# Kernel optimization log

Hardware: AMD Instinct MI355X
Metric: run time of the kernel (lower is better)

## Reference

```python
import jax, jax.numpy as jnp
import numpy as np

B, N, T, D, H, NE = 8, 128, 49, 4, 256, 2  # batch, nodes, timesteps, dims, hidden, edge types


def _mlp(x, w1, b1, w2, b2):
    # NRI-style 2-layer MLP with ELU activations (dropout=0, batch_norm off)
    h = jax.nn.elu(x @ w1 + b1)
    return jax.nn.elu(h @ w2 + b2)


def setup_inputs() -> dict:
    key = jax.random.key(0)
    ks = jax.random.split(key, 11)
    # fully-connected graph without self loops -> E = N*(N-1)
    off = ~np.eye(N, dtype=bool)
    recv_idx, send_idx = np.nonzero(off)
    eye = np.eye(N, dtype=np.float32)
    rec_rel = jnp.asarray(eye[recv_idx])   # [E, N] one-hot receivers
    send_rel = jnp.asarray(eye[send_idx])  # [E, N] one-hot senders
    x = jax.random.normal(ks[0], (B, N, T, D), jnp.float32)

    def lin(k, fi, fo):
        kw, kb = jax.random.split(k)
        return (0.02 * jax.random.normal(kw, (fi, fo), jnp.float32),
                0.02 * jax.random.normal(kb, (fo,), jnp.float32))

    F = T * D
    n1w1, n1b1 = lin(ks[1], F, H)
    n1w2, n1b2 = lin(ks[2], H, H)
    e1w1, e1b1 = lin(ks[3], 2 * H, H)
    e1w2, e1b2 = lin(ks[4], H, H)
    n2w1, n2b1 = lin(ks[5], H, H)
    n2w2, n2b2 = lin(ks[6], H, H)
    e2w1, e2b1 = lin(ks[7], 3 * H, H)
    e2w2, e2b2 = lin(ks[8], H, H)
    ow, ob = lin(ks[9], H, NE)
    return dict(x=x, rec_rel=rec_rel, send_rel=send_rel,
                n1w1=n1w1, n1b1=n1b1, n1w2=n1w2, n1b2=n1b2,
                e1w1=e1w1, e1b1=e1b1, e1w2=e1w2, e1b2=e1b2,
                n2w1=n2w1, n2b1=n2b1, n2w2=n2w2, n2b2=n2b2,
                e2w1=e2w1, e2b1=e2b1, e2w2=e2w2, e2b2=e2b2,
                ow=ow, ob=ob)


def reference(x, rec_rel, send_rel,
              n1w1, n1b1, n1w2, n1b2,
              e1w1, e1b1, e1w2, e1b2,
              n2w1, n2b1, n2w2, n2b2,
              e2w1, e2b1, e2w2, e2b2,
              ow, ob):
    b, n = x.shape[0], x.shape[1]
    h = x.reshape(b, n, -1)                         # [B, N, T*D]
    h = _mlp(h, n1w1, n1b1, n1w2, n1b2)             # node_emd 1 -> [B, N, H]
    r = jnp.einsum('en,bnf->bef', rec_rel, h)       # gather receivers [B, E, H]
    s = jnp.einsum('en,bnf->bef', send_rel, h)      # gather senders  [B, E, H]
    e = _mlp(jnp.concatenate([r, s], -1), e1w1, e1b1, e1w2, e1b2)  # edge_emd 1
    x_skip = e                                      # '@' skip connection
    agg = jnp.einsum('en,bef->bnf', rec_rel, e)     # aggregate sum -> [B, N, H]
    h = _mlp(agg, n2w1, n2b1, n2w2, n2b2)           # node_emd 2
    r = jnp.einsum('en,bnf->bef', rec_rel, h)
    s = jnp.einsum('en,bnf->bef', send_rel, h)
    e = jnp.concatenate([r, s, x_skip], -1)         # pairwise concat + residual cat
    e = _mlp(e, e2w1, e2b1, e2w2, e2b2)             # edge_emd 2 (final)
    return e @ ow + ob                              # [B, E, n_edge_types]
```

## Files before the change

### kernel.cpp

```cpp
#include <hip/hip_runtime.h>
#include <hip/hip_bf16.h>

typedef unsigned short ushort_t;
typedef short bf16x8 __attribute__((ext_vector_type(8)));
typedef float f32x4 __attribute__((ext_vector_type(4)));

#define B_ 8
#define N_ 128
#define E_ 16256
#define BE 130048

__device__ __forceinline__ float eluf(float x) {
    return x > 0.0f ? x : __expf(x) - 1.0f;
}
__device__ __forceinline__ ushort_t f2bf(float f) {
    union { float f; unsigned u; } v; v.f = f;
    return (ushort_t)((v.u + 0x7fffu + ((v.u >> 16) & 1u)) >> 16);
}

__device__ __forceinline__ void glds16(void* lds, const void* g) {
    __builtin_amdgcn_global_load_lds(
        (const __attribute__((address_space(1))) unsigned int*)g,
        (__attribute__((address_space(3))) unsigned int*)lds, 16, 0, 0);
}

__device__ __forceinline__ void img32_elem(const float* __restrict__ w,
                                           ushort_t* __restrict__ img, int i) {
    int c = i >> 13;  int r = i & 8191;
    int n = r >> 5;   int jq = r & 31;
    int quad = jq >> 3, j = jq & 7;
    int kc = quad ^ ((n >> 1) & 3);
    int k = c * 32 + kc * 8 + j;
    img[i] = f2bf(w[(size_t)k * 256 + n]);
}
__device__ __forceinline__ void img64_elem(const float* __restrict__ w,
                                           ushort_t* __restrict__ img, int i) {
    int c = i >> 14;  int r = i & 16383;
    int n = r >> 6;   int wdx = r & 63;
    int up = wdx >> 3, j = wdx & 7;
    int u = up ^ (n & 7);
    int k = c * 64 + u * 8 + j;
    img[i] = f2bf(w[(size_t)k * 256 + n]);
}
__device__ __forceinline__ void img128_elem(const float* __restrict__ w,
                                            ushort_t* __restrict__ img, int i) {
    int c = i >> 15;  int r = i & 32767;
    int n = r >> 7;   int wdx = r & 127;
    int up = wdx >> 3, j = wdx & 7;
    int u = up ^ (n & 15);
    int k = c * 128 + u * 8 + j;
    img[i] = f2bf(w[(size_t)k * 256 + n]);
}
__device__ __forceinline__ void img128_pad(const float* __restrict__ w,
                                           ushort_t* __restrict__ img, int i, int Kreal) {
    int c = i >> 15;  int r = i & 32767;
    int n = r >> 7;   int wdx = r & 127;
    int up = wdx >> 3, j = wdx & 7;
    int u = up ^ (n & 15);
    int k = c * 128 + u * 8 + j;
    img[i] = (k < Kreal) ? f2bf(w[(size_t)k * 256 + n]) : (ushort_t)0;
}

__global__ __launch_bounds__(256) void wprep_all(
    const float* __restrict__ n1w1, ushort_t* __restrict__ s0,
    const float* __restrict__ n1w2, ushort_t* __restrict__ s1,
    const float* __restrict__ e1w1, ushort_t* __restrict__ s2, ushort_t* __restrict__ s3,
    const float* __restrict__ n2w1, ushort_t* __restrict__ s4,
    const float* __restrict__ n2w2, ushort_t* __restrict__ s5,
    const float* __restrict__ e2w1, ushort_t* __restrict__ s6, ushort_t* __restrict__ s7,
    ushort_t* __restrict__ s8,
    const float* __restrict__ e1w2, ushort_t* __restrict__ s9,
    const float* __restrict__ e2w2, ushort_t* __restrict__ s10)
{
    int gid = blockIdx.x * 256 + threadIdx.x;
    int img = gid >> 16, r = gid & 65535;
    switch (img) {
        case 0:  img128_pad (n1w1, s0, r, 196); break;
        case 1:  img128_elem(n1w2, s1, r); break;
        case 2:  img128_elem(e1w1, s2, r); break;
        case 3:  img128_elem(e1w1 + 65536, s3, r); break;
        case 4:  img128_elem(n2w1, s4, r); break;
        case 5:  img128_elem(n2w2, s5, r); break;
        case 6:  img128_elem(e2w1, s6, r); break;
        case 7:  img128_elem(e2w1 + 65536, s7, r); break;
        case 8:  img64_elem (e2w1 + 131072, s8, r); break;
        case 9:  img32_elem (e1w2, s9, r); break;
        default: img32_elem (e2w2, s10, r); break;
    }
}

template<bool TWOIN>
__global__ __launch_bounds__(256, 1) void node_fused(
    const float* __restrict__ in0, const float* __restrict__ in1,
    const ushort_t* __restrict__ iw1, const float* __restrict__ b1,
    const ushort_t* __restrict__ iw2, const float* __restrict__ b2,
    const ushort_t* __restrict__ ipr, const ushort_t* __restrict__ ips,
    const float* __restrict__ bE,
    float* __restrict__ P)
{
    extern __shared__ char smem[];
    const int t = threadIdx.x;
    const int wid = t >> 6, lane = t & 63, lr = lane & 15, lg = lane >> 4;
    const int r0 = blockIdx.x * 32;

    float bias1[4], bias2[4], biasP[4];
    #pragma unroll
    for (int f = 0; f < 4; ++f) {
        int col = wid * 64 + f * 16 + lr;
        bias1[f] = b1[col];
        bias2[f] = b2[col];
        biasP[f] = 0.5f * bE[col];
    }

    f32x4 acc[2][4];
    #pragma unroll
    for (int m = 0; m < 2; ++m)
        #pragma unroll
        for (int f = 0; f < 4; ++f) acc[m][f] = f32x4{0.f, 0.f, 0.f, 0.f};

    auto stageW = [&](const ushort_t* img, int c, int p) {
        const char* src = (const char*)img + (size_t)c * 65536 + wid * 16384 + lane * 16;
        char* dst = smem + 16384 + p * 65536 + wid * 16384;
        #pragma unroll
        for (int it = 0; it < 16; ++it) glds16(dst + it * 1024, src + it * 1024);
    };

    int cc = 0;
    auto runGemm = [&](const ushort_t* img, const ushort_t* nimg) {
        for (int c = 0; c < 2; ++c) {
            const int p = cc & 1;
            if (c + 1 < 2)  stageW(img, 1, p ^ 1);
            else if (nimg)  stageW(nimg, 0, p ^ 1);
            const char* Wp = smem + 16384 + p * 65536;
            #pragma unroll
            for (int ks = 0; ks < 4; ++ks) {
                const int c32 = c * 4 + ks;
                bf16x8 a[2], b[4];
                const int qh = ((c32 * 4 + lg) ^ (lr & 7)) << 4;
                #pragma unroll
                for (int m = 0; m < 2; ++m)
                    a[m] = *(const bf16x8*)(smem + (m * 16 + lr) * 512 + qh);
                #pragma unroll
                for (int f = 0; f < 4; ++f)
                    b[f] = *(const bf16x8*)(Wp + (wid * 64 + f * 16 + lr) * 256 + (((ks * 4 + lg) ^ lr) << 4));
                #pragma unroll
                for (int m = 0; m < 2; ++m)
                    #pragma unroll
                    for (int f = 0; f < 4; ++f)
                        acc[m][f] = __builtin_amdgcn_mfma_f32_16x16x32_bf16(a[m], b[f], acc[m][f], 0, 0, 0);
            }
            __syncthreads();
            ++cc;
        }
    };

    auto transition = [&](const float* bv) {
        #pragma unroll
        for (int m = 0; m < 2; ++m)
            #pragma unroll
            for (int f = 0; f < 4; ++f) {
                const int col = wid * 64 + f * 16 + lr;
                const int ch = col >> 3;
                #pragma unroll
                for (int r = 0; r < 4; ++r) {
                    const int row = m * 16 + lg * 4 + r;
                    float v = eluf(acc[m][f][r] + bv[f]);
                    *(ushort_t*)(smem + row * 512 + ((ch ^ (row & 7)) << 4) + ((col & 7) << 1)) = f2bf(v);
                }
                acc[m][f] = f32x4{0.f, 0.f, 0.f, 0.f};
            }
        __syncthreads();
    };

    auto pwrite = [&](int half) {
        #pragma unroll
        for (int m = 0; m < 2; ++m)
            #pragma unroll
            for (int f = 0; f < 4; ++f) {
                const int col = wid * 64 + f * 16 + lr;
                #pragma unroll
                for (int r = 0; r < 4; ++r) {
                    const int row = m * 16 + lg * 4 + r;
                    P[(size_t)(r0 + row) * 512 + half * 256 + col] = acc[m][f][r] + biasP[f];
                }
                acc[m][f] = f32x4{0.f, 0.f, 0.f, 0.f};
            }
    };

    stageW(iw1, 0, 0);
    for (int idx = t; idx < 32 * 128; idx += 256) {
        const int row = idx >> 7;
        const int c0 = (idx & 127) * 2;
        float v0, v1;
        if (TWOIN) {
            const float* pa = in0 + (size_t)(r0 + row) * 256;
            const float* pb = in1 + (size_t)(r0 + row) * 256;
            v0 = pa[c0] + pb[c0];
            v1 = pa[c0 + 1] + pb[c0 + 1];
        } else {
            const float* pa = in0 + (size_t)(r0 + row) * 196;
            v0 = (c0 < 196) ? pa[c0] : 0.f;
            v1 = (c0 + 1 < 196) ? pa[c0 + 1] : 0.f;
        }
        unsigned u = (unsigned)f2bf(v0) | ((unsigned)f2bf(v1) << 16);
        const int ch = c0 >> 3;
        *(unsigned*)(smem + row * 512 + ((ch ^ (row & 7)) << 4) + (c0 & 7) * 2) = u;
    }
    __syncthreads();

    runGemm(iw1, iw2);
    transition(bias1);
    runGemm(iw2, ipr);
    transition(bias2);
    runGemm(ipr, ips);
    pwrite(0);
    runGemm(ips, nullptr);
    pwrite(1);
}

__global__ __launch_bounds__(512, 2) void edge1_kernel(
    const float* __restrict__ P1,
    const ushort_t* __restrict__ wimg, const float* __restrict__ bias,
    ushort_t* __restrict__ eout,
    float* __restrict__ aggp0, float* __restrict__ aggp1)
{
    extern __shared__ char smem[];
    const int t = threadIdx.x;
    const int wid = t >> 6, lane = t & 63, lr = lane & 15, lg = lane >> 4;
    const int wr = wid >> 1, wc = wid & 1;
    const int q4 = (lg ^ ((lr >> 1) & 3)) << 4;
    const int blockRow = blockIdx.x * 256;

    auto stageW = [&](int c, int p) {
        const char* src = (const char*)wimg + (size_t)c * 16384 + wid * 2048 + lane * 16;
        char* dst = smem + 131072 + p * 16384 + wid * 2048;
        glds16(dst, src);
        glds16(dst + 1024, src + 1024);
    };

    float biasA[8];
    #pragma unroll
    for (int f = 0; f < 8; ++f) biasA[f] = bias[wc * 128 + f * 16 + lr];

    f32x4 acc[4][8];
    #pragma unroll
    for (int m = 0; m < 4; ++m)
        #pragma unroll
        for (int f = 0; f < 8; ++f) acc[m][f] = f32x4{0.f, 0.f, 0.f, 0.f};

    stageW(0, 0);
    #pragma unroll 4
    for (int j = 0; j < 32; ++j) {
        const int row = wid * 32 + j;
        const int rg = blockRow + row;
        const int b = rg / E_; const int e = rg - b * E_;
        const int rcv = e / 127; const int kk = e - rcv * 127;
        const int snd = kk + (kk >= rcv ? 1 : 0);
        const float4 vr = *(const float4*)(P1 + (size_t)(b * N_ + rcv) * 512 + lane * 4);
        const float4 vs = *(const float4*)(P1 + (size_t)(b * N_ + snd) * 512 + 256 + lane * 4);
        unsigned u0 = (unsigned)f2bf(eluf(vr.x + vs.x)) | ((unsigned)f2bf(eluf(vr.y + vs.y)) << 16);
        unsigned u1 = (unsigned)f2bf(eluf(vr.z + vs.z)) | ((unsigned)f2bf(eluf(vr.w + vs.w)) << 16);
        const int byte = row * 512 + ((((lane >> 1) ^ (row & 7))) << 4) + (lane & 1) * 8;
        *(uint2*)(smem + byte) = make_uint2(u0, u1);
    }
    __syncthreads();

    for (int c = 0; c < 8; ++c) {
        const int p = c & 1;
        if (c < 7) stageW(c + 1, p ^ 1);
        const char* Wp = smem + 131072 + p * 16384;
        bf16x8 a[4], b[8];
        const int qh = ((c * 4 + lg) ^ (lr & 7)) << 4;
        #pragma unroll
        for (int m = 0; m < 4; ++m)
            a[m] = *(const bf16x8*)(smem + (wr * 64 + m * 16 + lr) * 512 + qh);
        #pragma unroll
        for (int f = 0; f < 8; ++f)
            b[f] = *(const bf16x8*)(Wp + (wc * 128 + f * 16 + lr) * 64 + q4);
        #pragma unroll
        for (int m = 0; m < 4; ++m)
            #pragma unroll
            for (int f = 0; f < 8; ++f)
                acc[m][f] = __builtin_amdgcn_mfma_f32_16x16x32_bf16(a[m], b[f], acc[m][f], 0, 0, 0);
        __syncthreads();
    }

    char* slice = smem + wid * 16384;
    const int gR0 = blockRow + wr * 64;
    const int sFirst = gR0 / 127;
    const int bk = 127 - (gR0 - sFirst * 127);
    float s0[8], s1[8];
    #pragma unroll
    for (int f = 0; f < 8; ++f) { s0[f] = 0.f; s1[f] = 0.f; }
    #pragma unroll
    for (int m = 0; m < 4; ++m)
        #pragma unroll
        for (int f = 0; f < 8; ++f) {
            const int col = f * 16 + lr;
            const int cc = col >> 3;
            #pragma unroll
            for (int r = 0; r < 4; ++r) {
                const int row = m * 16 + lg * 4 + r;
                float v = eluf(acc[m][f][r] + biasA[f]);
                *(ushort_t*)(slice + row * 256 + ((cc ^ (row & 7)) << 4) + ((col & 7) << 1)) = f2bf(v);
                if (row < bk) s0[f] += v; else s1[f] += v;
            }
        }
    #pragma unroll
    for (int f = 0; f < 8; ++f) {
        s0[f] += __shfl_xor(s0[f], 16); s0[f] += __shfl_xor(s0[f], 32);
        s1[f] += __shfl_xor(s1[f], 16); s1[f] += __shfl_xor(s1[f], 32);
    }
    float* pt = (float*)(smem + 131072);
    if (lg == 0) {
        #pragma unroll
        for (int f = 0; f < 8; ++f) {
            pt[(wid * 2 + 0) * 128 + f * 16 + lr] = s0[f];
            pt[(wid * 2 + 1) * 128 + f * 16 + lr] = s1[f];
        }
    }
    asm volatile("s_waitcnt lgkmcnt(0)" ::: "memory");
    #pragma unroll
    for (int it = 0; it < 16; ++it) {
        const int q = it * 64 + lane;
        const int row = q >> 4, ccp = q & 15;
        bf16x8 v = *(const bf16x8*)(slice + row * 256 + (ccp << 4));
        const int cc = ccp ^ (row & 7);
        const int grow = blockRow + wr * 64 + row;
        *(bf16x8*)(eout + (size_t)grow * 256 + wc * 128 + cc * 8) = v;
    }
    __syncthreads();
    const int S0 = blockRow / 127;
    const int last = (blockRow + 255) / 127;
    const int cnt = last - S0 + 1;
    for (int task = t; task < cnt * 256; task += 512) {
        const int k = task >> 8;
        const int col = task & 255;
        const int sigma = S0 + k;
        const int wcq = col >> 7, c128 = col & 127;
        float sum = 0.f;
        #pragma unroll
        for (int w2r = 0; w2r < 4; ++w2r) {
            int sf = (blockRow + w2r * 64) / 127;
            int jj = sigma - sf;
            if (jj == 0 || jj == 1)
                sum += pt[((w2r * 2 + wcq) * 2 + jj) * 128 + c128];
        }
        const bool startIn = (127 * sigma >= blockRow);
        const bool endIn = (127 * sigma + 127 <= blockRow + 256);
        if (startIn) {
            aggp0[(size_t)sigma * 256 + col] = sum;
            if (endIn) aggp1[(size_t)sigma * 256 + col] = 0.f;
        } else {
            aggp1[(size_t)sigma * 256 + col] = sum;
        }
    }
}

__global__ __launch_bounds__(512, 2) void edge2_kernel(
    const ushort_t* __restrict__ e1, const float* __restrict__ P2,
    const ushort_t* __restrict__ wBimg,
    const ushort_t* __restrict__ wCimg,
    const float* __restrict__ bC,
    const float* __restrict__ ow, const float* __restrict__ ob,
    float* __restrict__ out)
{
    extern __shared__ char smem[];
    const int t = threadIdx.x;
    const int wid = t >> 6, lane = t & 63, lr = lane & 15, lg = lane >> 4;
    const int wr = wid >> 1, wc = wid & 1;
    const int q4 = (lg ^ ((lr >> 1) & 3)) << 4;
    const int blockRow = blockIdx.x * 256;

    const int uoff = ((lane & 7) ^ ((lane >> 3) & 7)) * 8;
    const ushort_t* ap[4];
    #pragma unroll
    for (int it = 0; it < 4; ++it) {
        int r = wid * 32 + it * 8 + (lane >> 3);
        ap[it] = e1 + (size_t)(blockRow + r) * 256 + uoff;
    }

    float biasC[8];
    #pragma unroll
    for (int f = 0; f < 8; ++f) biasC[f] = bC[wc * 128 + f * 16 + lr];

    f32x4 acc[4][8];
    #pragma unroll
    for (int m = 0; m < 4; ++m)
        #pragma unroll
        for (int f = 0; f < 8; ++f) acc[m][f] = f32x4{0.f, 0.f, 0.f, 0.f};

    auto stageB64 = [&](int c, int p) {
        const char* src = (const char*)wBimg + (size_t)c * 32768 + wid * 4096 + lane * 16;
        char* dst = smem + 65536 + p * 32768 + wid * 4096;
        #pragma unroll
        for (int it = 0; it < 4; ++it) glds16(dst + it * 1024, src + it * 1024);
    };
    auto stageA64 = [&](int k0, int p) {
        char* dst = smem + p * 32768 + wid * 4096;
        #pragma unroll
        for (int it = 0; it < 4; ++it) glds16(dst + it * 1024, ap[it] + k0);
    };
    auto stageC = [&](int c, int p) {
        const char* src = (const char*)wCimg + (size_t)c * 16384 + wid * 2048 + lane * 16;
        char* dst = smem + 131072 + p * 16384 + wid * 2048;
        glds16(dst, src);
        glds16(dst + 1024, src + 1024);
    };

    stageB64(0, 0);
    stageA64(0, 0);
    __syncthreads();
    for (int c = 0; c < 4; ++c) {
        const int p = c & 1;
        if (c < 3) { stageB64(c + 1, p ^ 1); stageA64((c + 1) * 64, p ^ 1); }
        else       { stageC(0, 0); }
        const char* Ab = smem + p * 32768;
        const char* Bb = smem + 65536 + p * 32768;
        #pragma unroll
        for (int ks = 0; ks < 2; ++ks) {
            bf16x8 a[4], b[8];
            const int sw = ks * 4 + lg;
            #pragma unroll
            for (int m = 0; m < 4; ++m)
                a[m] = *(const bf16x8*)(Ab + (wr * 64 + m * 16 + lr) * 128 + ((sw ^ (lr & 7)) << 4));
            #pragma unroll
            for (int f = 0; f < 8; ++f)
                b[f] = *(const bf16x8*)(Bb + (wc * 128 + f * 16 + lr) * 128 + ((sw ^ (lr & 7)) << 4));
            #pragma unroll
            for (int m = 0; m < 4; ++m)
                #pragma unroll
                for (int f = 0; f < 8; ++f)
                    acc[m][f] = __builtin_amdgcn_mfma_f32_16x16x32_bf16(a[m], b[f], acc[m][f], 0, 0, 0);
        }
        __syncthreads();
    }

    #pragma unroll
    for (int m = 0; m < 4; ++m)
        #pragma unroll
        for (int r = 0; r < 4; ++r) {
            const int row = wr * 64 + m * 16 + lg * 4 + r;
            const int rg = blockRow + row;
            const int b = rg / E_; const int e = rg - b * E_;
            const int rcv = e / 127; const int kk = e - rcv * 127;
            const int snd = kk + (kk >= rcv ? 1 : 0);
            const float* pr = P2 + (size_t)(b * N_ + rcv) * 512;
            const float* ps = P2 + (size_t)(b * N_ + snd) * 512 + 256;
            #pragma unroll
            for (int f = 0; f < 8; ++f) {
                const int col = wc * 128 + f * 16 + lr;
                float v = eluf(acc[m][f][r] + pr[col] + ps[col]);
                const int ch = col >> 3;
                *(ushort_t*)(smem + row * 512 + ((ch ^ (row & 7)) << 4) + ((col & 7) << 1)) = f2bf(v);
            }
        }
    #pragma unroll
    for (int m = 0; m < 4; ++m)
        #pragma unroll
        for (int f = 0; f < 8; ++f) acc[m][f] = f32x4{0.f, 0.f, 0.f, 0.f};
    __syncthreads();

    for (int c = 0; c < 8; ++c) {
        const int p = c & 1;
        if (c < 7) stageC(c + 1, p ^ 1);
        const char* Wp = smem + 131072 + p * 16384;
        bf16x8 a[4], b[8];
        const int qh = ((c * 4 + lg) ^ (lr & 7)) << 4;
        #pragma unroll
        for (int m = 0; m < 4; ++m)
            a[m] = *(const bf16x8*)(smem + (wr * 64 + m * 16 + lr) * 512 + qh);
        #pragma unroll
        for (int f = 0; f < 8; ++f)
            b[f] = *(const bf16x8*)(Wp + (wc * 128 + f * 16 + lr) * 64 + q4);
        #pragma unroll
        for (int m = 0; m < 4; ++m)
            #pragma unroll
            for (int f = 0; f < 8; ++f)
                acc[m][f] = __builtin_amdgcn_mfma_f32_16x16x32_bf16(a[m], b[f], acc[m][f], 0, 0, 0);
        __syncthreads();
    }

    float ow0[8], ow1[8];
    #pragma unroll
    for (int f = 0; f < 8; ++f) {
        int col = wc * 128 + f * 16 + lr;
        ow0[f] = ow[col * 2 + 0];
        ow1[f] = ow[col * 2 + 1];
    }
    float s0[4][4], s1[4][4];
    #pragma unroll
    for (int m = 0; m < 4; ++m)
        #pragma unroll
        for (int r = 0; r < 4; ++r) { s0[m][r] = 0.f; s1[m][r] = 0.f; }
    #pragma unroll
    for (int m = 0; m < 4; ++m)
        #pragma unroll
        for (int f = 0; f < 8; ++f)
            #pragma unroll
            for (int r = 0; r < 4; ++r) {
                float v = eluf(acc[m][f][r] + biasC[f]);
                s0[m][r] = fmaf(v, ow0[f], s0[m][r]);
                s1[m][r] = fmaf(v, ow1[f], s1[m][r]);
            }
    #pragma unroll
    for (int msk = 1; msk <= 8; msk <<= 1)
        #pragma unroll
        for (int m = 0; m < 4; ++m)
            #pragma unroll
            for (int r = 0; r < 4; ++r) {
                s0[m][r] += __shfl_xor(s0[m][r], msk);
                s1[m][r] += __shfl_xor(s1[m][r], msk);
            }
    float* part = (float*)smem;
    if (lr == 0) {
        #pragma unroll
        for (int m = 0; m < 4; ++m)
            #pragma unroll
            for (int r = 0; r < 4; ++r) {
                const int row = wr * 64 + m * 16 + lg * 4 + r;
                part[(row * 2 + 0) * 2 + wc] = s0[m][r];
                part[(row * 2 + 1) * 2 + wc] = s1[m][r];
            }
    }
    __syncthreads();
    const int row = t >> 1, chn = t & 1;
    float val = part[(row * 2 + chn) * 2 + 0] + part[(row * 2 + chn) * 2 + 1] + ob[chn];
    out[(size_t)(blockRow + row) * 2 + chn] = val;
}

extern "C" void kernel_launch(void* const* d_in, const int* in_sizes, int n_in,
                              void* d_out, int out_size, void* d_ws, size_t ws_size,
                              hipStream_t stream)
{
    const float* x    = (const float*)d_in[0];
    const float* n1w1 = (const float*)d_in[3];
    const float* n1b1 = (const float*)d_in[4];
    const float* n1w2 = (const float*)d_in[5];
    const float* n1b2 = (const float*)d_in[6];
    const float* e1w1 = (const float*)d_in[7];
    const float* e1b1 = (const float*)d_in[8];
    const float* e1w2 = (const float*)d_in[9];
    const float* e1b2 = (const float*)d_in[10];
    const float* n2w1 = (const float*)d_in[11];
    const float* n2b1 = (const float*)d_in[12];
    const float* n2w2 = (const float*)d_in[13];
    const float* n2b2 = (const float*)d_in[14];
    const float* e2w1 = (const float*)d_in[15];
    const float* e2b1 = (const float*)d_in[16];
    const float* e2w2 = (const float*)d_in[17];
    const float* e2b2 = (const float*)d_in[18];
    const float* ow   = (const float*)d_in[19];
    const float* ob   = (const float*)d_in[20];

    char* ws = (char*)d_ws;
    const size_t KB = 1024;
    ushort_t* i_n1w1 = (ushort_t*)(ws + 0 * 128 * KB);
    ushort_t* i_n1w2 = (ushort_t*)(ws + 1 * 128 * KB);
    ushort_t* i_p1r  = (ushort_t*)(ws + 2 * 128 * KB);
    ushort_t* i_p1s  = (ushort_t*)(ws + 3 * 128 * KB);
    ushort_t* i_n2w1 = (ushort_t*)(ws + 4 * 128 * KB);
    ushort_t* i_n2w2 = (ushort_t*)(ws + 5 * 128 * KB);
    ushort_t* i_p2r  = (ushort_t*)(ws + 6 * 128 * KB);
    ushort_t* i_p2s  = (ushort_t*)(ws + 7 * 128 * KB);
    ushort_t* wB     = (ushort_t*)(ws + 8 * 128 * KB);
    ushort_t* wA     = (ushort_t*)(ws + 9 * 128 * KB);
    ushort_t* wC     = (ushort_t*)(ws + 10 * 128 * KB);
    float*    P1    = (float*)(ws + 1536 * KB);
    float*    P2    = (float*)(ws + 1536 * KB + (2u << 20));
    float*    aggp0 = (float*)(ws + 1536 * KB + (4u << 20));
    float*    aggp1 = (float*)(ws + 1536 * KB + (5u << 20));
    ushort_t* e1    = (ushort_t*)(ws + 1536 * KB + (6u << 20));

    float* out = (float*)d_out;

    hipFuncSetAttribute((const void*)node_fused<false>,
                        hipFuncAttributeMaxDynamicSharedMemorySize, 147456);
    hipFuncSetAttribute((const void*)node_fused<true>,
                        hipFuncAttributeMaxDynamicSharedMemorySize, 147456);
    hipFuncSetAttribute((const void*)edge1_kernel,
                        hipFuncAttributeMaxDynamicSharedMemorySize, 163840);
    hipFuncSetAttribute((const void*)edge2_kernel,
                        hipFuncAttributeMaxDynamicSharedMemorySize, 163840);

    wprep_all<<<2816, 256, 0, stream>>>(
        n1w1, i_n1w1, n1w2, i_n1w2, e1w1, i_p1r, i_p1s,
        n2w1, i_n2w1, n2w2, i_n2w2, e2w1, i_p2r, i_p2s, wB,
        e1w2, wA, e2w2, wC);

    node_fused<false><<<32, 256, 147456, stream>>>(
        x, nullptr, i_n1w1, n1b1, i_n1w2, n1b2, i_p1r, i_p1s, e1b1, P1);

    edge1_kernel<<<BE / 256, 512, 163840, stream>>>(P1, wA, e1b2, e1, aggp0, aggp1);

    node_fused<true><<<32, 256, 147456, stream>>>(
        aggp0, aggp1, i_n2w1, n2b1, i_n2w2, n2b2, i_p2r, i_p2s, e2b1, P2);

    edge2_kernel<<<BE / 256, 512, 163840, stream>>>(
        e1, P2, wB, wC, e2b2, ow, ob, out);
}
```

Measured before the change: 160.9 us.

## Move skip-connection GEMM into edge1 kernel and pass bf16 partial product to edge2

```diff
diff --git a/kernel.cpp b/kernel.cpp
--- a/kernel.cpp
+++ b/kernel.cpp
@@ -16,6 +16,10 @@
 __device__ __forceinline__ ushort_t f2bf(float f) {
     union { float f; unsigned u; } v; v.f = f;
     return (ushort_t)((v.u + 0x7fffu + ((v.u >> 16) & 1u)) >> 16);
+}
+__device__ __forceinline__ float bf2f(ushort_t h) {
+    union { unsigned u; float f; } v; v.u = ((unsigned)h) << 16;
+    return v.f;
 }
 
 __device__ __forceinline__ void glds16(void* lds, const void* g) {
@@ -31,15 +35,6 @@
     int quad = jq >> 3, j = jq & 7;
     int kc = quad ^ ((n >> 1) & 3);
     int k = c * 32 + kc * 8 + j;
-    img[i] = f2bf(w[(size_t)k * 256 + n]);
-}
-__device__ __forceinline__ void img64_elem(const float* __restrict__ w,
-                                           ushort_t* __restrict__ img, int i) {
-    int c = i >> 14;  int r = i & 16383;
-    int n = r >> 6;   int wdx = r & 63;
-    int up = wdx >> 3, j = wdx & 7;
-    int u = up ^ (n & 7);
-    int k = c * 64 + u * 8 + j;
     img[i] = f2bf(w[(size_t)k * 256 + n]);
 }
 __device__ __forceinline__ void img128_elem(const float* __restrict__ w,
@@ -83,7 +78,7 @@
         case 5:  img128_elem(n2w2, s5, r); break;
         case 6:  img128_elem(e2w1, s6, r); break;
         case 7:  img128_elem(e2w1 + 65536, s7, r); break;
-        case 8:  img64_elem (e2w1 + 131072, s8, r); break;
+        case 8:  img32_elem (e2w1 + 131072, s8, r); break;
         case 9:  img32_elem (e1w2, s9, r); break;
         default: img32_elem (e2w2, s10, r); break;
     }
@@ -220,8 +215,9 @@
 
 __global__ __launch_bounds__(512, 2) void edge1_kernel(
     const float* __restrict__ P1,
-    const ushort_t* __restrict__ wimg, const float* __restrict__ bias,
-    ushort_t* __restrict__ eout,
+    const ushort_t* __restrict__ wAimg, const float* __restrict__ biasA,
+    const ushort_t* __restrict__ wBimg,
+    ushort_t* __restrict__ G1,
     float* __restrict__ aggp0, float* __restrict__ aggp1)
 {
     extern __shared__ char smem[];
@@ -231,16 +227,16 @@
     const int q4 = (lg ^ ((lr >> 1) & 3)) << 4;
     const int blockRow = blockIdx.x * 256;
 
-    auto stageW = [&](int c, int p) {
-        const char* src = (const char*)wimg + (size_t)c * 16384 + wid * 2048 + lane * 16;
+    auto stageW = [&](const ushort_t* img, int c, int p) {
+        const char* src = (const char*)img + (size_t)c * 16384 + wid * 2048 + lane * 16;
         char* dst = smem + 131072 + p * 16384 + wid * 2048;
         glds16(dst, src);
         glds16(dst + 1024, src + 1024);
     };
 
-    float biasA[8];
-    #pragma unroll
-    for (int f = 0; f < 8; ++f) biasA[f] = bias[wc * 128 + f * 16 + lr];
+    float bA[8];
+    #pragma unroll
+    for (int f = 0; f < 8; ++f) bA[f] = biasA[wc * 128 + f * 16 + lr];
 
     f32x4 acc[4][8];
     #pragma unroll
@@ -248,7 +244,7 @@
         #pragma unroll
         for (int f = 0; f < 8; ++f) acc[m][f] = f32x4{0.f, 0.f, 0.f, 0.f};
 
-    stageW(0, 0);
+    stageW(wAimg, 0, 0);
     #pragma unroll 4
     for (int j = 0; j < 32; ++j) {
         const int row = wid * 32 + j;
@@ -267,7 +263,8 @@
 
     for (int c = 0; c < 8; ++c) {
         const int p = c & 1;
-        if (c < 7) stageW(c + 1, p ^ 1);
+        if (c < 7) stageW(wAimg, c + 1, p ^ 1);
+        else       stageW(wBimg, 0, p ^ 1);
         const char* Wp = smem + 131072 + p * 16384;
         bf16x8 a[4], b[8];
         const int qh = ((c * 4 + lg) ^ (lr & 7)) << 4;
@@ -285,7 +282,6 @@
         __syncthreads();
     }
 
-    char* slice = smem + wid * 16384;
     const int gR0 = blockRow + wr * 64;
     const int sFirst = gR0 / 127;
     const int bk = 127 - (gR0 - sFirst * 127);
@@ -296,22 +292,24 @@
     for (int m = 0; m < 4; ++m)
         #pragma unroll
         for (int f = 0; f < 8; ++f) {
-            const int col = f * 16 + lr;
-            const int cc = col >> 3;
+            const int col = wc * 128 + f * 16 + lr;
+            const int ch = col >> 3;
             #pragma unroll
             for (int r = 0; r < 4; ++r) {
-                const int row = m * 16 + lg * 4 + r;
-                float v = eluf(acc[m][f][r] + biasA[f]);
-                *(ushort_t*)(slice + row * 256 + ((cc ^ (row & 7)) << 4) + ((col & 7) << 1)) = f2bf(v);
-                if (row < bk) s0[f] += v; else s1[f] += v;
-            }
+                const int rowL = m * 16 + lg * 4 + r;
+                const int row = wr * 64 + rowL;
+                float v = eluf(acc[m][f][r] + bA[f]);
+                *(ushort_t*)(smem + row * 512 + ((ch ^ (row & 7)) << 4) + ((col & 7) << 1)) = f2bf(v);
+                if (rowL < bk) s0[f] += v; else s1[f] += v;
+            }
+            acc[m][f] = f32x4{0.f, 0.f, 0.f, 0.f};
         }
     #pragma unroll
     for (int f = 0; f < 8; ++f) {
         s0[f] += __shfl_xor(s0[f], 16); s0[f] += __shfl_xor(s0[f], 32);
         s1[f] += __shfl_xor(s1[f], 16); s1[f] += __shfl_xor(s1[f], 32);
     }
-    float* pt = (float*)(smem + 131072);
+    float* pt = (float*)(smem + 131072 + 16384);
     if (lg == 0) {
         #pragma unroll
         for (int f = 0; f < 8; ++f) {
@@ -319,49 +317,85 @@
             pt[(wid * 2 + 1) * 128 + f * 16 + lr] = s1[f];
         }
     }
+    __syncthreads();
+    {
+        const int S0 = blockRow / 127;
+        const int last = (blockRow + 255) / 127;
+        const int cnt = last - S0 + 1;
+        for (int task = t; task < cnt * 256; task += 512) {
+            const int k = task >> 8;
+            const int col = task & 255;
+            const int sigma = S0 + k;
+            const int wcq = col >> 7, c128 = col & 127;
+            float sum = 0.f;
+            #pragma unroll
+            for (int w2r = 0; w2r < 4; ++w2r) {
+                int sf = (blockRow + w2r * 64) / 127;
+                int jj = sigma - sf;
+                if (jj == 0 || jj == 1)
+                    sum += pt[((w2r * 2 + wcq) * 2 + jj) * 128 + c128];
+            }
+            const bool startIn = (127 * sigma >= blockRow);
+            const bool endIn = (127 * sigma + 127 <= blockRow + 256);
+            if (startIn) {
+                aggp0[(size_t)sigma * 256 + col] = sum;
+                if (endIn) aggp1[(size_t)sigma * 256 + col] = 0.f;
+            } else {
+                aggp1[(size_t)sigma * 256 + col] = sum;
+            }
+        }
+    }
+    __syncthreads();
+
+    for (int c = 0; c < 8; ++c) {
+        const int p = c & 1;
+        if (c < 7) stageW(wBimg, c + 1, p ^ 1);
+        const char* Wp = smem + 131072 + p * 16384;
+        bf16x8 a[4], b[8];
+        const int qh = ((c * 4 + lg) ^ (lr & 7)) << 4;
+        #pragma unroll
+        for (int m = 0; m < 4; ++m)
+            a[m] = *(const bf16x8*)(smem + (wr * 64 + m * 16 + lr) * 512 + qh);
+        #pragma unroll
+        for (int f = 0; f < 8; ++f)
+            b[f] = *(const bf16x8*)(Wp + (wc * 128 + f * 16 + lr) * 64 + q4);
+        #pragma unroll
+        for (int m = 0; m < 4; ++m)
+            #pragma unroll
+            for (int f = 0; f < 8; ++f)
+                acc[m][f] = __builtin_amdgcn_mfma_f32_16x16x32_bf16(a[m], b[f], acc[m][f], 0, 0, 0);
+        __syncthreads();
+    }
+
+    char* slice = smem + wid * 16384;
+    #pragma unroll
+    for (int m = 0; m < 4; ++m)
+        #pragma unroll
+        for (int f = 0; f < 8; ++f) {
+            const int col = f * 16 + lr;
+            const int cch = col >> 3;
+            #pragma unroll
+            for (int r = 0; r < 4; ++r) {
+                const int rowL = m * 16 + lg * 4 + r;
+                *(ushort_t*)(slice + rowL * 256 + ((cch ^ (rowL & 7)) << 4) + ((col & 7) << 1)) =
+                    f2bf(acc[m][f][r]);
+            }
+        }
     asm volatile("s_waitcnt lgkmcnt(0)" ::: "memory");
     #pragma unroll
     for (int it = 0; it < 16; ++it) {
         const int q = it * 64 + lane;
         const int row = q >> 4, ccp = q & 15;
         bf16x8 v = *(const bf16x8*)(slice + row * 256 + (ccp << 4));
-        const int cc = ccp ^ (row & 7);
+        const int cch = ccp ^ (row & 7);
         const int grow = blockRow + wr * 64 + row;
-        *(bf16x8*)(eout + (size_t)grow * 256 + wc * 128 + cc * 8) = v;
-    }
-    __syncthreads();
-    const int S0 = blockRow / 127;
-    const int last = (blockRow + 255) / 127;
-    const int cnt = last - S0 + 1;
-    for (int task = t; task < cnt * 256; task += 512) {
-        const int k = task >> 8;
-        const int col = task & 255;
-        const int sigma = S0 + k;
-        const int wcq = col >> 7, c128 = col & 127;
-        float sum = 0.f;
-        #pragma unroll
-        for (int w2r = 0; w2r < 4; ++w2r) {
-            int sf = (blockRow + w2r * 64) / 127;
-            int jj = sigma - sf;
-            if (jj == 0 || jj == 1)
-                sum += pt[((w2r * 2 + wcq) * 2 + jj) * 128 + c128];
-        }
-        const bool startIn = (127 * sigma >= blockRow);
-        const bool endIn = (127 * sigma + 127 <= blockRow + 256);
-        if (startIn) {
-            aggp0[(size_t)sigma * 256 + col] = sum;
-            if (endIn) aggp1[(size_t)sigma * 256 + col] = 0.f;
-        } else {
-            aggp1[(size_t)sigma * 256 + col] = sum;
-        }
+        *(bf16x8*)(G1 + (size_t)grow * 256 + wc * 128 + cch * 8) = v;
     }
 }
 
 __global__ __launch_bounds__(512, 2) void edge2_kernel(
-    const ushort_t* __restrict__ e1, const float* __restrict__ P2,
-    const ushort_t* __restrict__ wBimg,
-    const ushort_t* __restrict__ wCimg,
-    const float* __restrict__ bC,
+    const ushort_t* __restrict__ G1, const float* __restrict__ P2,
+    const ushort_t* __restrict__ wCimg, const float* __restrict__ bC,
     const float* __restrict__ ow, const float* __restrict__ ob,
     float* __restrict__ out)
 {
@@ -372,98 +406,46 @@
     const int q4 = (lg ^ ((lr >> 1) & 3)) << 4;
     const int blockRow = blockIdx.x * 256;
 
-    const int uoff = ((lane & 7) ^ ((lane >> 3) & 7)) * 8;
-    const ushort_t* ap[4];
-    #pragma unroll
-    for (int it = 0; it < 4; ++it) {
-        int r = wid * 32 + it * 8 + (lane >> 3);
-        ap[it] = e1 + (size_t)(blockRow + r) * 256 + uoff;
-    }
-
-    float biasC[8];
-    #pragma unroll
-    for (int f = 0; f < 8; ++f) biasC[f] = bC[wc * 128 + f * 16 + lr];
-
-    f32x4 acc[4][8];
-    #pragma unroll
-    for (int m = 0; m < 4; ++m)
-        #pragma unroll
-        for (int f = 0; f < 8; ++f) acc[m][f] = f32x4{0.f, 0.f, 0.f, 0.f};
-
-    auto stageB64 = [&](int c, int p) {
-        const char* src = (const char*)wBimg + (size_t)c * 32768 + wid * 4096 + lane * 16;
-        char* dst = smem + 65536 + p * 32768 + wid * 4096;
-        #pragma unroll
-        for (int it = 0; it < 4; ++it) glds16(dst + it * 1024, src + it * 1024);
-    };
-    auto stageA64 = [&](int k0, int p) {
-        char* dst = smem + p * 32768 + wid * 4096;
-        #pragma unroll
-        for (int it = 0; it < 4; ++it) glds16(dst + it * 1024, ap[it] + k0);
-    };
-    auto stageC = [&](int c, int p) {
+    auto stageW = [&](int c, int p) {
         const char* src = (const char*)wCimg + (size_t)c * 16384 + wid * 2048 + lane * 16;
         char* dst = smem + 131072 + p * 16384 + wid * 2048;
         glds16(dst, src);
         glds16(dst + 1024, src + 1024);
     };
 
-    stageB64(0, 0);
-    stageA64(0, 0);
-    __syncthreads();
-    for (int c = 0; c < 4; ++c) {
-        const int p = c & 1;
-        if (c < 3) { stageB64(c + 1, p ^ 1); stageA64((c + 1) * 64, p ^ 1); }
-        else       { stageC(0, 0); }
-        const char* Ab = smem + p * 32768;
-        const char* Bb = smem + 65536 + p * 32768;
-        #pragma unroll
-        for (int ks = 0; ks < 2; ++ks) {
-            bf16x8 a[4], b[8];
-            const int sw = ks * 4 + lg;
-            #pragma unroll
-            for (int m = 0; m < 4; ++m)
-                a[m] = *(const bf16x8*)(Ab + (wr * 64 + m * 16 + lr) * 128 + ((sw ^ (lr & 7)) << 4));
-            #pragma unroll
-            for (int f = 0; f < 8; ++f)
-                b[f] = *(const bf16x8*)(Bb + (wc * 128 + f * 16 + lr) * 128 + ((sw ^ (lr & 7)) << 4));
-            #pragma unroll
-            for (int m = 0; m < 4; ++m)
-                #pragma unroll
-                for (int f = 0; f < 8; ++f)
-                    acc[m][f] = __builtin_amdgcn_mfma_f32_16x16x32_bf16(a[m], b[f], acc[m][f], 0, 0, 0);
-        }
-        __syncthreads();
-    }
-
+    float biasC[8];
+    #pragma unroll
+    for (int f = 0; f < 8; ++f) biasC[f] = bC[wc * 128 + f * 16 + lr];
+
+    f32x4 acc[4][8];
     #pragma unroll
     for (int m = 0; m < 4; ++m)
         #pragma unroll
-        for (int r = 0; r < 4; ++r) {
-            const int row = wr * 64 + m * 16 + lg * 4 + r;
-            const int rg = blockRow + row;
-            const int b = rg / E_; const int e = rg - b * E_;
-            const int rcv = e / 127; const int kk = e - rcv * 127;
-            const int snd = kk + (kk >= rcv ? 1 : 0);
-            const float* pr = P2 + (size_t)(b * N_ + rcv) * 512;
-            const float* ps = P2 + (size_t)(b * N_ + snd) * 512 + 256;
-            #pragma unroll
-            for (int f = 0; f < 8; ++f) {
-                const int col = wc * 128 + f * 16 + lr;
-                float v = eluf(acc[m][f][r] + pr[col] + ps[col]);
-                const int ch = col >> 3;
-                *(ushort_t*)(smem + row * 512 + ((ch ^ (row & 7)) << 4) + ((col & 7) << 1)) = f2bf(v);
-            }
-        }
-    #pragma unroll
-    for (int m = 0; m < 4; ++m)
-        #pragma unroll
         for (int f = 0; f < 8; ++f) acc[m][f] = f32x4{0.f, 0.f, 0.f, 0.f};
+
+    stageW(0, 0);
+    #pragma unroll 4
+    for (int j = 0; j < 32; ++j) {
+        const int row = wid * 32 + j;
+        const int rg = blockRow + row;
+        const int b = rg / E_; const int e = rg - b * E_;
+        const int rcv = e / 127; const int kk = e - rcv * 127;
+        const int snd = kk + (kk >= rcv ? 1 : 0);
+        const ushort4 g4 = *(const ushort4*)(G1 + (size_t)rg * 256 + lane * 4);
+        const float4 vr = *(const float4*)(P2 + (size_t)(b * N_ + rcv) * 512 + lane * 4);
+        const float4 vs = *(const float4*)(P2 + (size_t)(b * N_ + snd) * 512 + 256 + lane * 4);
+        unsigned u0 = (unsigned)f2bf(eluf(bf2f(g4.x) + vr.x + vs.x))
+                    | ((unsigned)f2bf(eluf(bf2f(g4.y) + vr.y + vs.y)) << 16);
+        unsigned u1 = (unsigned)f2bf(eluf(bf2f(g4.z) + vr.z + vs.z))
+                    | ((unsigned)f2bf(eluf(bf2f(g4.w) + vr.w + vs.w)) << 16);
+        const int byte = row * 512 + ((((lane >> 1) ^ (row & 7))) << 4) + (lane & 1) * 8;
+        *(uint2*)(smem + byte) = make_uint2(u0, u1);
+    }
     __syncthreads();
 
     for (int c = 0; c < 8; ++c) {
         const int p = c & 1;
-        if (c < 7) stageC(c + 1, p ^ 1);
+        if (c < 7) stageW(c + 1, p ^ 1);
         const char* Wp = smem + 131072 + p * 16384;
         bf16x8 a[4], b[8];
         const int qh = ((c * 4 + lg) ^ (lr & 7)) << 4;
@@ -570,7 +552,7 @@
     float*    P2    = (float*)(ws + 1536 * KB + (2u << 20));
     float*    aggp0 = (float*)(ws + 1536 * KB + (4u << 20));
     float*    aggp1 = (float*)(ws + 1536 * KB + (5u << 20));
-    ushort_t* e1    = (ushort_t*)(ws + 1536 * KB + (6u << 20));
+    ushort_t* G1    = (ushort_t*)(ws + 1536 * KB + (6u << 20));
 
     float* out = (float*)d_out;
 
@@ -591,11 +573,12 @@
     node_fused<false><<<32, 256, 147456, stream>>>(
         x, nullptr, i_n1w1, n1b1, i_n1w2, n1b2, i_p1r, i_p1s, e1b1, P1);
 
-    edge1_kernel<<<BE / 256, 512, 163840, stream>>>(P1, wA, e1b2, e1, aggp0, aggp1);
+    edge1_kernel<<<BE / 256, 512, 163840, stream>>>(
+        P1, wA, e1b2, wB, G1, aggp0, aggp1);
 
     node_fused<true><<<32, 256, 147456, stream>>>(
         aggp0, aggp1, i_n2w1, n2b1, i_n2w2, n2b2, i_p2r, i_p2s, e2b1, P2);
 
     edge2_kernel<<<BE / 256, 512, 163840, stream>>>(
-        e1, P2, wB, wC, e2b2, ow, ob, out);
-}
+        G1, P2, wC, e2b2, ow, ob, out);
+}
```

After: 161.6 us. Within noise of the previous version (+0.4%).
